# Optimization experiments

Measured on AMD Instinct MI355X. Metric: run time of the kernel, lower is better.

The kernel has to match this reference:

```python
import jax, jax.numpy as jnp
import numpy as np
from jax import lax

KH = 5
KW = 5


def dwconv3x3(x, w, b):
    # depthwise 3x3, padding 1; w: (C,1,3,3), b: (C,)
    C = x.shape[1]
    y = lax.conv_general_dilated(x, w, (1, 1), ((1, 1), (1, 1)),
                                 feature_group_count=C,
                                 dimension_numbers=('NCHW', 'OIHW', 'NCHW'))
    return y + b[None, :, None, None]


def conv3x3(x, w, b):
    y = lax.conv_general_dilated(x, w, (1, 1), ((1, 1), (1, 1)),
                                 dimension_numbers=('NCHW', 'OIHW', 'NCHW'))
    return y + b[None, :, None, None]


def resize_bilinear_ac(x, H, W):
    # bilinear, align_corners=True (matches F.interpolate(..., align_corners=True))
    N, C, h, w = x.shape
    ys = jnp.linspace(0.0, h - 1.0, H)
    xs = jnp.linspace(0.0, w - 1.0, W)
    y0 = jnp.floor(ys).astype(jnp.int32)
    x0 = jnp.floor(xs).astype(jnp.int32)
    y1 = jnp.clip(y0 + 1, 0, h - 1)
    x1 = jnp.clip(x0 + 1, 0, w - 1)
    wy = (ys - y0)[None, None, :, None]
    wx = (xs - x0)[None, None, None, :]
    rows = x[:, :, y0, :] * (1.0 - wy) + x[:, :, y1, :] * wy  # (N,C,H,w)
    out = rows[:, :, :, x0] * (1.0 - wx) + rows[:, :, :, x1] * wx  # (N,C,H,W)
    return out


def unfold_kxk(x, kH, kW):
    # torch.nn.Unfold(kernel=(kH,kW), padding=(kH//2,kW//2)) reshaped to (N,C,kH*kW,H,W)
    N, C, H, W = x.shape
    ph, pw = kH // 2, kW // 2
    xp = jnp.pad(x, ((0, 0), (0, 0), (ph, ph), (pw, pw)))
    patches = [xp[:, :, i:i + H, j:j + W] for i in range(kH) for j in range(kW)]
    return jnp.stack(patches, axis=2)  # (N,C,kH*kW,H,W), row-major window order


def setup_inputs() -> dict:
    key = jax.random.key(0)
    ks = jax.random.split(key, 11)
    N, C, H, W = 2, 128, 128, 128
    s = 1.0 / np.sqrt(9.0)
    return {
        'hr_feat': jax.random.normal(ks[0], (N, C, H, W), jnp.float32),
        'lr_feat': jax.random.normal(ks[1], (N, C, H // 2, W // 2), jnp.float32),
        'wq': jax.random.normal(ks[2], (C, 1, 3, 3), jnp.float32) * s,
        'bq': jax.random.normal(ks[3], (C,), jnp.float32) * 0.02,
        'wk': jax.random.normal(ks[4], (C, 1, 3, 3), jnp.float32) * s,
        'bk': jax.random.normal(ks[5], (C,), jnp.float32) * 0.02,
        'wv': jax.random.normal(ks[6], (C, 1, 3, 3), jnp.float32) * s,
        'bv': jax.random.normal(ks[7], (C,), jnp.float32) * 0.02,
        'wa': jax.random.normal(ks[8], (2, 2 * C, 3, 3), jnp.float32) * (1.0 / np.sqrt(9.0 * 2 * C)),
        'ba': jax.random.normal(ks[9], (2,), jnp.float32) * 0.02,
    }


def reference(hr_feat, lr_feat, wq, bq, wk, bk, wv, bv, wa, ba):
    N, C, H, W = hr_feat.shape
    lr_up = resize_bilinear_ac(lr_feat, H, W)
    hr_value = dwconv3x3(hr_feat, wv, bv)
    hr_key = dwconv3x3(hr_feat, wk, bk)
    lr_query = dwconv3x3(lr_up, wq, bq)
    fused = jnp.concatenate([lr_query, hr_key], axis=1)
    dyn = jax.nn.sigmoid(conv3x3(fused, wa, ba))  # (N,2,H,W)
    k_unf = unfold_kxk(hr_key, KH, KW)            # (N,C,K,H,W)
    sim = jnp.einsum('nchw,nckhw->nkhw', lr_query, k_unf)
    weight = jax.nn.softmax(sim, axis=1)          # softmax over window K
    v_unf = unfold_kxk(hr_value, KH, KW)
    attn = dyn[:, 0:1] * jnp.einsum('nckhw,nkhw->nchw', v_unf, weight)
    attn = attn + dyn[:, 1:2] * hr_value
    return lr_up + attn
```

## Files before the change

### kernel.cpp

```cpp
#include <hip/hip_runtime.h>
#include <hip/hip_fp16.h>
#include <math.h>

constexpr int C  = 128;
constexpr int H  = 128;
constexpr int Wd = 128;
constexpr int HW = H * Wd;
constexpr int LH = 64, LW = 64;
constexpr int CP = 64;

constexpr int KRW = 136;
constexpr int KPLANE = 132 * KRW;
constexpr int QRW = 136;
constexpr int QPLANE = 130 * QRW;
constexpr int KSZ = 2 * CP * KPLANE;
constexpr int QSZ = 2 * CP * QPLANE;
constexpr int LSZ = 2 * CP * HW;
constexpr int WAHSZ = 2304;

typedef _Float16 __attribute__((ext_vector_type(2))) v2h;

#if __has_builtin(__builtin_amdgcn_fdot2)
#define DOT2(a, b, c) __builtin_amdgcn_fdot2((a), (b), (c), false)
#else
#define DOT2(a, b, c) ((c) + (float)(a).x * (float)(b).x + (float)(a).y * (float)(b).y)
#endif

struct __attribute__((packed, aligned(4)))  f4u { float x, y, z, w; };
struct __attribute__((packed, aligned(4)))  f4p { v2h a, b, c, d; };
struct __attribute__((packed, aligned(8)))  h2x2 { v2h a, b; };
struct __attribute__((packed, aligned(16))) h4 { v2h a, b, c, d; };

__device__ __forceinline__ v2h pack2(float a, float b) {
  v2h r; r.x = (_Float16)a; r.y = (_Float16)b; return r;
}

__global__ __launch_bounds__(256) void k_pre(
    const float* __restrict__ hr, const float* __restrict__ lr,
    const float* __restrict__ wq, const float* __restrict__ bq,
    const float* __restrict__ wk, const float* __restrict__ bk,
    const float* __restrict__ wv, const float* __restrict__ bv,
    const float* __restrict__ wa,
    v2h* __restrict__ qpad, v2h* __restrict__ kpad, v2h* __restrict__ vpad,
    v2h* __restrict__ lrup, v2h* __restrict__ zgapA, v2h* __restrict__ zgapB,
    v2h* __restrict__ wah)
{
  const int B   = blockIdx.x;
  const int tid = threadIdx.x;
  const int t   = B * 256 + tid;
  const int q   = B & 7;
  const int m   = B >> 3;
  const int j   = (q << 1) | (m & 1);
  const int ncp = m >> 1;
  const int x4  = tid & 31;
  const int y   = (j << 3) | ((tid >> 5) & 7);
  const int x   = x4 * 4;
  const int cp  = ncp & (CP - 1);
  const int n   = ncp >> 6;
  const int c0  = cp * 2;
  const v2h hz  = pack2(0.f, 0.f);
  h4 Z; Z.a = hz; Z.b = hz; Z.c = hz; Z.d = hz;

  if (t < WAHSZ) {
    const int cpw = t / 36, r = t - cpw * 36;
    const int o = r / 18, s2 = (r - o * 18) / 9, tap = r - o * 18 - s2 * 9;
    const int c = s2 * 128 + 2 * cpw;
    wah[t] = pack2(wa[(o * 256 + c) * 9 + tap], wa[(o * 256 + c + 1) * 9 + tap]);
  }

  float ko[2][4], vo[2][4];
#pragma unroll
  for (int cc = 0; cc < 2; cc++) {
    const int c = c0 + cc;
    const float* hp = hr + (n * C + c) * HW;
    const float* wkc = wk + c * 9;
    const float* wvc = wv + c * 9;
    const float bkc = bk[c], bvc = bv[c];
#pragma unroll
    for (int jj = 0; jj < 4; jj++) { ko[cc][jj] = bkc; vo[cc][jj] = bvc; }
#pragma unroll
    for (int r = 0; r < 3; r++) {
      const int gy = y + r - 1;
      const bool okr = (gy >= 0) && (gy < H);
      const int gyc = min(max(gy, 0), H - 1);
      const float* rp = hp + gyc * Wd;
      const f4u mm = *(const f4u*)(rp + x);
      const float lft = rp[max(x - 1, 0)];
      const float rgt = rp[min(x + 4, Wd - 1)];
      float h[6];
      h[0] = (okr && x > 0) ? lft : 0.f;
      h[1] = okr ? mm.x : 0.f;  h[2] = okr ? mm.y : 0.f;
      h[3] = okr ? mm.z : 0.f;  h[4] = okr ? mm.w : 0.f;
      h[5] = (okr && x + 4 < Wd) ? rgt : 0.f;
#pragma unroll
      for (int dj = 0; dj < 3; dj++) {
        const float a = wkc[r * 3 + dj], b = wvc[r * 3 + dj];
#pragma unroll
        for (int jj = 0; jj < 4; jj++) {
          ko[cc][jj] += a * h[jj + dj];
          vo[cc][jj] += b * h[jj + dj];
        }
      }
    }
  }

  v2h* kr = kpad + ncp * KPLANE + (y + 2) * KRW + 4 + x;
  v2h* vr = vpad + ncp * KPLANE + (y + 2) * KRW + 4 + x;
  {
    h4 K4; K4.a = pack2(ko[0][0], ko[1][0]); K4.b = pack2(ko[0][1], ko[1][1]);
           K4.c = pack2(ko[0][2], ko[1][2]); K4.d = pack2(ko[0][3], ko[1][3]);
    h4 V4; V4.a = pack2(vo[0][0], vo[1][0]); V4.b = pack2(vo[0][1], vo[1][1]);
           V4.c = pack2(vo[0][2], vo[1][2]); V4.d = pack2(vo[0][3], vo[1][3]);
    *(h4*)(kr) = K4;
    *(h4*)(vr) = V4;
  }

  const float s = 63.0f / 127.0f;

  float rwm[3][3]; int rA[3];
  {
    int ry0[3]; float wyv[3]; bool okr[3];
#pragma unroll
    for (int r = 0; r < 3; r++) {
      const int gy = y + r - 1;
      okr[r] = (gy >= 0) && (gy < H);
      const int gyc = min(max(gy, 0), H - 1);
      const float fy = gyc * s;
      const int y0 = (int)fy;
      ry0[r] = y0;
      wyv[r] = fy - y0;
    }
    const int Y = ry0[0];
#pragma unroll
    for (int tt = 0; tt < 3; tt++) rA[tt] = min(Y + tt, LH - 1) * LW;
#pragma unroll
    for (int r = 0; r < 3; r++) {
      const int i0 = ry0[r] - Y;
      const int i1 = min(ry0[r] + 1, LH - 1) - Y;
#pragma unroll
      for (int tt = 0; tt < 3; tt++) {
        const float w = ((tt == i0) ? (1.f - wyv[r]) : 0.f)
                      + ((tt == i1) ? wyv[r] : 0.f);
        rwm[r][tt] = okr[r] ? w : 0.f;
      }
    }
  }

  float cwm[6][5]; int XB;
  {
    int cx0[6]; float wxv[6]; bool okc[6];
#pragma unroll
    for (int jj = 0; jj < 6; jj++) {
      const int gx = x + jj - 1;
      okc[jj] = (gx >= 0) && (gx < Wd);
      const int gxc = min(max(gx, 0), Wd - 1);
      const float fx = gxc * s;
      const int x0 = (int)fx;
      cx0[jj] = x0;
      wxv[jj] = fx - x0;
    }
    XB = min(cx0[0], LW - 5);
#pragma unroll
    for (int jj = 0; jj < 6; jj++) {
      const int i0 = cx0[jj] - XB;
      const int i1 = min(cx0[jj] + 1, LW - 1) - XB;
#pragma unroll
      for (int u = 0; u < 5; u++) {
        const float w = ((u == i0) ? (1.f - wxv[jj]) : 0.f)
                      + ((u == i1) ? wxv[jj] : 0.f);
        cwm[jj][u] = okc[jj] ? w : 0.f;
      }
    }
  }

  float qo[2][4], up[2][4];
#pragma unroll
  for (int cc = 0; cc < 2; cc++) {
    const int c = c0 + cc;
    const float* lp = lr + (n * C + c) * (LH * LW);
    const float* wqc = wq + c * 9;
    const float bqc = bq[c];
#pragma unroll
    for (int jj = 0; jj < 4; jj++) qo[cc][jj] = bqc;

    float R[3][5];
#pragma unroll
    for (int tt = 0; tt < 3; tt++) {
      const f4u mm = *(const f4u*)(lp + rA[tt] + XB);
      R[tt][0] = mm.x; R[tt][1] = mm.y; R[tt][2] = mm.z; R[tt][3] = mm.w;
      R[tt][4] = lp[rA[tt] + XB + 4];
    }

    float yi[3][5];
#pragma unroll
    for (int r = 0; r < 3; r++)
#pragma unroll
      for (int u = 0; u < 5; u++)
        yi[r][u] = rwm[r][0] * R[0][u] + rwm[r][1] * R[1][u]
                 + rwm[r][2] * R[2][u];

#pragma unroll
    for (int r = 0; r < 3; r++) {
      float row[6];
#pragma unroll
      for (int jj = 0; jj < 6; jj++)
        row[jj] = cwm[jj][0] * yi[r][0] + cwm[jj][1] * yi[r][1]
               + cwm[jj][2] * yi[r][2] + cwm[jj][3] * yi[r][3]
               + cwm[jj][4] * yi[r][4];
#pragma unroll
      for (int dj = 0; dj < 3; dj++) {
        const float a = wqc[r * 3 + dj];
#pragma unroll
        for (int jj = 0; jj < 4; jj++) qo[cc][jj] += a * row[jj + dj];
      }
      if (r == 1) {
        up[cc][0] = row[1]; up[cc][1] = row[2];
        up[cc][2] = row[3]; up[cc][3] = row[4];
      }
    }
  }

  {
    h4 U;
    U.a = pack2(up[0][0], up[1][0]); U.b = pack2(up[0][1], up[1][1]);
    U.c = pack2(up[0][2], up[1][2]); U.d = pack2(up[0][3], up[1][3]);
    *(h4*)(lrup + ncp * HW + y * Wd + x) = U;
  }
  v2h* qr = qpad + ncp * QPLANE + (y + 1) * QRW + 4 + x;
  {
    h4 Q4; Q4.a = pack2(qo[0][0], qo[1][0]); Q4.b = pack2(qo[0][1], qo[1][1]);
           Q4.c = pack2(qo[0][2], qo[1][2]); Q4.d = pack2(qo[0][3], qo[1][3]);
    *(h4*)(qr) = Q4;
  }

  if (x4 == 0) {
    *(h4*)(kr - 4) = Z; *(h4*)(vr - 4) = Z; *(h4*)(qr - 4) = Z;
  }
  if (x4 == 31) {
    *(h4*)(kr + 4) = Z; *(h4*)(vr + 4) = Z; *(h4*)(qr + 4) = Z;
  }
  if (y == 0) {
    v2h* kz = kpad + ncp * KPLANE;
    v2h* vz = vpad + ncp * KPLANE;
    v2h* qz = qpad + ncp * QPLANE;
    *(h4*)(kz + 4 + x) = Z; *(h4*)(kz + KRW + 4 + x) = Z;
    *(h4*)(vz + 4 + x) = Z; *(h4*)(vz + KRW + 4 + x) = Z;
    *(h4*)(qz + 4 + x) = Z;
    if (x4 == 0) {
      *(h4*)(kz) = Z; *(h4*)(kz + KRW) = Z;
      *(h4*)(vz) = Z; *(h4*)(vz + KRW) = Z;
      *(h4*)(qz) = Z;
    }
    if (x4 == 31) {
      *(h4*)(kz + 132) = Z; *(h4*)(kz + KRW + 132) = Z;
      *(h4*)(vz + 132) = Z; *(h4*)(vz + KRW + 132) = Z;
      *(h4*)(qz + 132) = Z;
    }
  }
  if (y == 127) {
    v2h* kz = kpad + ncp * KPLANE + 130 * KRW;
    v2h* vz = vpad + ncp * KPLANE + 130 * KRW;
    v2h* qz = qpad + ncp * QPLANE + 129 * QRW;
    *(h4*)(kz + 4 + x) = Z; *(h4*)(kz + KRW + 4 + x) = Z;
    *(h4*)(vz + 4 + x) = Z; *(h4*)(vz + KRW + 4 + x) = Z;
    *(h4*)(qz + 4 + x) = Z;
    if (x4 == 0) {
      *(h4*)(kz) = Z; *(h4*)(kz + KRW) = Z;
      *(h4*)(vz) = Z; *(h4*)(vz + KRW) = Z;
      *(h4*)(qz) = Z;
    }
    if (x4 == 31) {
      *(h4*)(kz + 132) = Z; *(h4*)(kz + KRW + 132) = Z;
      *(h4*)(vz + 132) = Z; *(h4*)(vz + KRW + 132) = Z;
      *(h4*)(qz + 132) = Z;
    }
  }
  if (t < 256) zgapA[t] = hz;
  if (t < 4)   zgapB[t] = hz;
}

#define DECLK(P, kp) \
  const f4p P##A0 = *(const f4p*)(kp); \
  const f4p P##A1 = *(const f4p*)((kp) + KRW); \
  const f4p P##A2 = *(const f4p*)((kp) + 2 * KRW); \
  const f4p P##A3 = *(const f4p*)((kp) + 3 * KRW); \
  const f4p P##A4 = *(const f4p*)((kp) + 4 * KRW); \
  const v2h P##b0 = (kp)[4]; \
  const v2h P##b1 = (kp)[KRW + 4]; \
  const v2h P##b2 = (kp)[2 * KRW + 4]; \
  const v2h P##b3 = (kp)[3 * KRW + 4]; \
  const v2h P##b4 = (kp)[4 * KRW + 4];

#define DECLQ(P, qp) \
  const f4p P##Q0 = *(const f4p*)(qp); \
  const f4p P##Q1 = *(const f4p*)((qp) + QRW); \
  const f4p P##Q2 = *(const f4p*)((qp) + 2 * QRW);

#define SIM25(P, qc) \
  sim[0]  = DOT2(qc, P##A0.a, sim[0]);  sim[1]  = DOT2(qc, P##A0.b, sim[1]); \
  sim[2]  = DOT2(qc, P##A0.c, sim[2]);  sim[3]  = DOT2(qc, P##A0.d, sim[3]); \
  sim[4]  = DOT2(qc, P##b0,   sim[4]); \
  sim[5]  = DOT2(qc, P##A1.a, sim[5]);  sim[6]  = DOT2(qc, P##A1.b, sim[6]); \
  sim[7]  = DOT2(qc, P##A1.c, sim[7]);  sim[8]  = DOT2(qc, P##A1.d, sim[8]); \
  sim[9]  = DOT2(qc, P##b1,   sim[9]); \
  sim[10] = DOT2(qc, P##A2.a, sim[10]); sim[11] = DOT2(qc, P##A2.b, sim[11]); \
  sim[12] = DOT2(qc, P##A2.c, sim[12]); sim[13] = DOT2(qc, P##A2.d, sim[13]); \
  sim[14] = DOT2(qc, P##b2,   sim[14]); \
  sim[15] = DOT2(qc, P##A3.a, sim[15]); sim[16] = DOT2(qc, P##A3.b, sim[16]); \
  sim[17] = DOT2(qc, P##A3.c, sim[17]); sim[18] = DOT2(qc, P##A3.d, sim[18]); \
  sim[19] = DOT2(qc, P##b3,   sim[19]); \
  sim[20] = DOT2(qc, P##A4.a, sim[20]); sim[21] = DOT2(qc, P##A4.b, sim[21]); \
  sim[22] = DOT2(qc, P##A4.c, sim[22]); sim[23] = DOT2(qc, P##A4.d, sim[23]); \
  sim[24] = DOT2(qc, P##b4,   sim[24]);

#define GATE(P, wp) { \
  const v2h q3_[9] = {P##Q0.a, P##Q0.b, P##Q0.c, P##Q1.a, P##Q1.b, P##Q1.c, \
                      P##Q2.a, P##Q2.b, P##Q2.c}; \
  const v2h k3_[9] = {P##A1.b, P##A1.c, P##A1.d, P##A2.b, P##A2.c, P##A2.d, \
                      P##A3.b, P##A3.c, P##A3.d}; \
  _Pragma("unroll") \
  for (int tp = 0; tp < 9; tp++) { \
    d0a = DOT2((wp)[tp],      q3_[tp], d0a); \
    d0a = DOT2((wp)[9 + tp],  k3_[tp], d0a); \
    d1a = DOT2((wp)[18 + tp], q3_[tp], d1a); \
    d1a = DOT2((wp)[27 + tp], k3_[tp], d1a); \
  } }

#define EPI(P, ci) { \
  v2h accA = wpk[0] * P##A0.a; \
  accA += wpk[1]  * P##A0.b;  accA += wpk[2]  * P##A0.c; \
  accA += wpk[3]  * P##A0.d;  accA += wpk[4]  * P##b0; \
  v2h accB = wpk[5] * P##A1.a; \
  accB += wpk[6]  * P##A1.b;  accB += wpk[7]  * P##A1.c; \
  accB += wpk[8]  * P##A1.d;  accB += wpk[9]  * P##b1; \
  accA += wpk[10] * P##A2.a;  accA += wpk[11] * P##A2.b; \
  accA += wpk[12] * P##A2.c;  accA += wpk[13] * P##A2.d; \
  accA += wpk[14] * P##b2; \
  accB += wpk[15] * P##A3.a;  accB += wpk[16] * P##A3.b; \
  accB += wpk[17] * P##A3.c;  accB += wpk[18] * P##A3.d; \
  accB += wpk[19] * P##b3; \
  accA += wpk[20] * P##A4.a;  accA += wpk[21] * P##A4.b; \
  accA += wpk[22] * P##A4.c;  accA += wpk[23] * P##A4.d; \
  accA += wpk[24] * P##b4; \
  const float acc0 = (float)accA.x + (float)accB.x; \
  const float acc1 = (float)accA.y + (float)accB.y; \
  const v2h vc = P##A2.c; \
  const v2h lu = lub[(ci) * HW]; \
  float* op = opb + (ci) * 2 * HW; \
  op[0]  = (float)lu.x + g0 * acc0 + g1 * (float)vc.x; \
  op[HW] = (float)lu.y + g0 * acc1 + g1 * (float)vc.y; }

__global__ __launch_bounds__(1024, 4) void k_attn(
    const v2h* __restrict__ qpad, const v2h* __restrict__ kpad,
    const v2h* __restrict__ vpad, const v2h* __restrict__ lrup,
    const v2h* __restrict__ wah, const float* __restrict__ ba,
    float* __restrict__ outb)
{
  __shared__ float red[25 * 1024];
  __shared__ float dsh[2 * 1024];

  const int tid = threadIdx.x;
  const int px  = tid & 63;
  const int cgu = __builtin_amdgcn_readfirstlane((tid >> 6) & 7);
  const int row = __builtin_amdgcn_readfirstlane(tid >> 9);
  const int slot = blockIdx.x;
  const int xcd = slot & 7;
  const int m   = slot >> 3;
  const int y   = (xcd << 4) + ((m & 7) << 1) + row;
  const int x   = ((m >> 3) & 1) * 64 + px;
  const int n   = m >> 4;
  const int cp0 = cgu * 8;

  const float ba0 = ba[0], ba1 = ba[1];

  const v2h* kb = kpad + (n * CP + cp0) * KPLANE + y * KRW + 2 + x;
  const v2h* qb = qpad + (n * CP + cp0) * QPLANE + y * QRW + 3 + x;

  float sim[25];
#pragma unroll
  for (int k = 0; k < 25; k++) sim[k] = 0.f;
  float d0a = 0.f, d1a = 0.f;

#pragma unroll
  for (int cib = 0; cib < 8; cib += 2) {
    const v2h* kp0 = kb + cib * KPLANE;
    const v2h* kp1 = kp0 + KPLANE;
    const v2h* qp0 = qb + cib * QPLANE;
    const v2h* qp1 = qp0 + QPLANE;

    DECLK(S, kp0)
    DECLK(T, kp1)
    DECLQ(S, qp0)

    const v2h qc0 = SQ1.b;
    SIM25(S, qc0)
    GATE(S, wah + (cp0 + cib) * 36)

    DECLQ(T, qp1)
    const v2h qc1 = TQ1.b;
    SIM25(T, qc1)
    GATE(T, wah + (cp0 + cib + 1) * 36)
  }

#pragma unroll
  for (int k = 0; k < 25; k++) red[k * 1024 + tid] = sim[k];
  dsh[tid] = d0a;
  dsh[1024 + tid] = d1a;
  __syncthreads();

  {
    const int w = tid >> 6;
    for (int s = w; s < 54; s += 16) {
      if (s < 50) {
        const int k = s >> 1, r = s & 1;
        float acc = 0.f;
#pragma unroll
        for (int g = 0; g < 8; g++) acc += red[k * 1024 + r * 512 + g * 64 + px];
        red[k * 1024 + r * 512 + px] = acc;
      } else {
        const int jj = s - 50;
        const int r = jj & 1, which = jj >> 1;
        float acc = 0.f;
#pragma unroll
        for (int g = 0; g < 8; g++) acc += dsh[which * 1024 + r * 512 + g * 64 + px];
        dsh[which * 1024 + r * 512 + px] = acc;
      }
    }
  }
  __syncthreads();

  const v2h* vb = vpad + (n * CP + cp0) * KPLANE + y * KRW + 2 + x;
  const v2h* lub = lrup + (n * CP + cp0) * HW + y * Wd + x;
  float* opb = outb + (n * C + 2 * cp0) * HW + y * Wd + x;

  DECLK(VA, vb)
  DECLK(VB, vb + KPLANE)

  const int rbase = row * 512 + px;
  float w[25];
  float mx = -1e30f;
#pragma unroll
  for (int k = 0; k < 25; k++) { w[k] = red[k * 1024 + rbase]; mx = fmaxf(mx, w[k]); }
  float tot = 0.f;
#pragma unroll
  for (int k = 0; k < 25; k++) { const float e = __expf(w[k] - mx); w[k] = e; tot += e; }
  const float inv = __builtin_amdgcn_rcpf(tot);
  v2h wpk[25];
#pragma unroll
  for (int k = 0; k < 25; k++) {
    const float wf = w[k] * inv;
    wpk[k] = pack2(wf, wf);
  }
  const float g0 = __builtin_amdgcn_rcpf(1.f + __expf(-(dsh[rbase] + ba0)));
  const float g1 = __builtin_amdgcn_rcpf(1.f + __expf(-(dsh[1024 + rbase] + ba1)));

  EPI(VA, 0)
  EPI(VB, 1)

#pragma unroll
  for (int cib = 2; cib < 8; cib += 2) {
    DECLK(VC, vb + cib * KPLANE)
    DECLK(VD, vb + (cib + 1) * KPLANE)
    EPI(VC, cib)
    EPI(VD, cib + 1)
  }
}

extern "C" void kernel_launch(void* const* d_in, const int* in_sizes, int n_in,
                              void* d_out, int out_size, void* d_ws,
                              size_t ws_size, hipStream_t stream)
{
  const float* hr = (const float*)d_in[0];
  const float* lr = (const float*)d_in[1];
  const float* wq = (const float*)d_in[2];
  const float* bq = (const float*)d_in[3];
  const float* wk = (const float*)d_in[4];
  const float* bk = (const float*)d_in[5];
  const float* wv = (const float*)d_in[6];
  const float* bv = (const float*)d_in[7];
  const float* wa = (const float*)d_in[8];
  const float* ba = (const float*)d_in[9];

  float* out = (float*)d_out;
  v2h* ws2 = (v2h*)d_ws;

  v2h* kpad  = ws2;
  v2h* vpad  = kpad + KSZ;
  v2h* qpad  = vpad + KSZ;
  v2h* zgapA = qpad + QSZ;
  v2h* lrupb = zgapA + 256;
  v2h* zgapB = lrupb + LSZ;
  v2h* wahb  = zgapB + 4;

  k_pre<<<dim3(2048), dim3(256), 0, stream>>>(
      hr, lr, wq, bq, wk, bk, wv, bv, wa,
      qpad, kpad, vpad, lrupb, zgapA, zgapB, wahb);
  k_attn<<<dim3(256), dim3(1024), 0, stream>>>(
      qpad, kpad, vpad, lrupb, wahb, ba, out);
}
```

Before: 118.1 us.

## Fuse key/value depthwise convs into attention kernel via shared-memory staging

Removes the key and value depthwise 3x3 convolutions from the pre-pass and their padded fp16 global buffers. The attention kernel now computes them directly from hr into an LDS tile with halo, first for keys and then for values, reusing the same buffer. The cross-channel-group reduction of sim and gate partials now uses LDS atomicAdd into a small buffer instead of a large staging array and a tree pass. This cuts global writes and reads of the K/V intermediates. In exchange, each block recomputes halo rows and columns, and the conv work plus atomic contention now sit inside the attention kernel's critical path.

```diff
diff --git a/kernel.cpp b/kernel.cpp
--- a/kernel.cpp
+++ b/kernel.cpp
@@ -9,14 +9,13 @@
 constexpr int LH = 64, LW = 64;
 constexpr int CP = 64;
 
-constexpr int KRW = 136;
-constexpr int KPLANE = 132 * KRW;
 constexpr int QRW = 136;
 constexpr int QPLANE = 130 * QRW;
-constexpr int KSZ = 2 * CP * KPLANE;
 constexpr int QSZ = 2 * CP * QPLANE;
 constexpr int LSZ = 2 * CP * HW;
 constexpr int WAHSZ = 2304;
+
+constexpr int KVSTR = 433;
 
 typedef _Float16 __attribute__((ext_vector_type(2))) v2h;
 
@@ -28,7 +27,6 @@
 
 struct __attribute__((packed, aligned(4)))  f4u { float x, y, z, w; };
 struct __attribute__((packed, aligned(4)))  f4p { v2h a, b, c, d; };
-struct __attribute__((packed, aligned(8)))  h2x2 { v2h a, b; };
 struct __attribute__((packed, aligned(16))) h4 { v2h a, b, c, d; };
 
 __device__ __forceinline__ v2h pack2(float a, float b) {
@@ -36,13 +34,11 @@
 }
 
 __global__ __launch_bounds__(256) void k_pre(
-    const float* __restrict__ hr, const float* __restrict__ lr,
+    const float* __restrict__ lr,
     const float* __restrict__ wq, const float* __restrict__ bq,
-    const float* __restrict__ wk, const float* __restrict__ bk,
-    const float* __restrict__ wv, const float* __restrict__ bv,
     const float* __restrict__ wa,
-    v2h* __restrict__ qpad, v2h* __restrict__ kpad, v2h* __restrict__ vpad,
-    v2h* __restrict__ lrup, v2h* __restrict__ zgapA, v2h* __restrict__ zgapB,
+    v2h* __restrict__ qpad, v2h* __restrict__ lrup,
+    v2h* __restrict__ zgapA, v2h* __restrict__ zgapB,
     v2h* __restrict__ wah)
 {
   const int B   = blockIdx.x;
@@ -68,53 +64,6 @@
     wah[t] = pack2(wa[(o * 256 + c) * 9 + tap], wa[(o * 256 + c + 1) * 9 + tap]);
   }
 
-  float ko[2][4], vo[2][4];
-#pragma unroll
-  for (int cc = 0; cc < 2; cc++) {
-    const int c = c0 + cc;
-    const float* hp = hr + (n * C + c) * HW;
-    const float* wkc = wk + c * 9;
-    const float* wvc = wv + c * 9;
-    const float bkc = bk[c], bvc = bv[c];
-#pragma unroll
-    for (int jj = 0; jj < 4; jj++) { ko[cc][jj] = bkc; vo[cc][jj] = bvc; }
-#pragma unroll
-    for (int r = 0; r < 3; r++) {
-      const int gy = y + r - 1;
-      const bool okr = (gy >= 0) && (gy < H);
-      const int gyc = min(max(gy, 0), H - 1);
-      const float* rp = hp + gyc * Wd;
-      const f4u mm = *(const f4u*)(rp + x);
-      const float lft = rp[max(x - 1, 0)];
-      const float rgt = rp[min(x + 4, Wd - 1)];
-      float h[6];
-      h[0] = (okr && x > 0) ? lft : 0.f;
-      h[1] = okr ? mm.x : 0.f;  h[2] = okr ? mm.y : 0.f;
-      h[3] = okr ? mm.z : 0.f;  h[4] = okr ? mm.w : 0.f;
-      h[5] = (okr && x + 4 < Wd) ? rgt : 0.f;
-#pragma unroll
-      for (int dj = 0; dj < 3; dj++) {
-        const float a = wkc[r * 3 + dj], b = wvc[r * 3 + dj];
-#pragma unroll
-        for (int jj = 0; jj < 4; jj++) {
-          ko[cc][jj] += a * h[jj + dj];
-          vo[cc][jj] += b * h[jj + dj];
-        }
-      }
-    }
-  }
-
-  v2h* kr = kpad + ncp * KPLANE + (y + 2) * KRW + 4 + x;
-  v2h* vr = vpad + ncp * KPLANE + (y + 2) * KRW + 4 + x;
-  {
-    h4 K4; K4.a = pack2(ko[0][0], ko[1][0]); K4.b = pack2(ko[0][1], ko[1][1]);
-           K4.c = pack2(ko[0][2], ko[1][2]); K4.d = pack2(ko[0][3], ko[1][3]);
-    h4 V4; V4.a = pack2(vo[0][0], vo[1][0]); V4.b = pack2(vo[0][1], vo[1][1]);
-           V4.c = pack2(vo[0][2], vo[1][2]); V4.d = pack2(vo[0][3], vo[1][3]);
-    *(h4*)(kr) = K4;
-    *(h4*)(vr) = V4;
-  }
-
   const float s = 63.0f / 127.0f;
 
   float rwm[3][3]; int rA[3];
@@ -233,63 +182,33 @@
     *(h4*)(qr) = Q4;
   }
 
-  if (x4 == 0) {
-    *(h4*)(kr - 4) = Z; *(h4*)(vr - 4) = Z; *(h4*)(qr - 4) = Z;
-  }
-  if (x4 == 31) {
-    *(h4*)(kr + 4) = Z; *(h4*)(vr + 4) = Z; *(h4*)(qr + 4) = Z;
-  }
+  if (x4 == 0)  { *(h4*)(qr - 4) = Z; }
+  if (x4 == 31) { *(h4*)(qr + 4) = Z; }
   if (y == 0) {
-    v2h* kz = kpad + ncp * KPLANE;
-    v2h* vz = vpad + ncp * KPLANE;
     v2h* qz = qpad + ncp * QPLANE;
-    *(h4*)(kz + 4 + x) = Z; *(h4*)(kz + KRW + 4 + x) = Z;
-    *(h4*)(vz + 4 + x) = Z; *(h4*)(vz + KRW + 4 + x) = Z;
     *(h4*)(qz + 4 + x) = Z;
-    if (x4 == 0) {
-      *(h4*)(kz) = Z; *(h4*)(kz + KRW) = Z;
-      *(h4*)(vz) = Z; *(h4*)(vz + KRW) = Z;
-      *(h4*)(qz) = Z;
-    }
-    if (x4 == 31) {
-      *(h4*)(kz + 132) = Z; *(h4*)(kz + KRW + 132) = Z;
-      *(h4*)(vz + 132) = Z; *(h4*)(vz + KRW + 132) = Z;
-      *(h4*)(qz + 132) = Z;
-    }
+    if (x4 == 0)  { *(h4*)(qz) = Z; }
+    if (x4 == 31) { *(h4*)(qz + 132) = Z; }
   }
   if (y == 127) {
-    v2h* kz = kpad + ncp * KPLANE + 130 * KRW;
-    v2h* vz = vpad + ncp * KPLANE + 130 * KRW;
     v2h* qz = qpad + ncp * QPLANE + 129 * QRW;
-    *(h4*)(kz + 4 + x) = Z; *(h4*)(kz + KRW + 4 + x) = Z;
-    *(h4*)(vz + 4 + x) = Z; *(h4*)(vz + KRW + 4 + x) = Z;
     *(h4*)(qz + 4 + x) = Z;
-    if (x4 == 0) {
-      *(h4*)(kz) = Z; *(h4*)(kz + KRW) = Z;
-      *(h4*)(vz) = Z; *(h4*)(vz + KRW) = Z;
-      *(h4*)(qz) = Z;
-    }
-    if (x4 == 31) {
-      *(h4*)(kz + 132) = Z; *(h4*)(kz + KRW + 132) = Z;
-      *(h4*)(vz + 132) = Z; *(h4*)(vz + KRW + 132) = Z;
-      *(h4*)(qz + 132) = Z;
-    }
+    if (x4 == 0)  { *(h4*)(qz) = Z; }
+    if (x4 == 31) { *(h4*)(qz + 132) = Z; }
   }
   if (t < 256) zgapA[t] = hz;
   if (t < 4)   zgapB[t] = hz;
 }
 
-#define DECLK(P, kp) \
-  const f4p P##A0 = *(const f4p*)(kp); \
-  const f4p P##A1 = *(const f4p*)((kp) + KRW); \
-  const f4p P##A2 = *(const f4p*)((kp) + 2 * KRW); \
-  const f4p P##A3 = *(const f4p*)((kp) + 3 * KRW); \
-  const f4p P##A4 = *(const f4p*)((kp) + 4 * KRW); \
-  const v2h P##b0 = (kp)[4]; \
-  const v2h P##b1 = (kp)[KRW + 4]; \
-  const v2h P##b2 = (kp)[2 * KRW + 4]; \
-  const v2h P##b3 = (kp)[3 * KRW + 4]; \
-  const v2h P##b4 = (kp)[4 * KRW + 4];
+#define DECLK_L(P, kb_) \
+  f4p P##A0, P##A1, P##A2, P##A3, P##A4; \
+  v2h P##b0, P##b1, P##b2, P##b3, P##b4; \
+  { const v2h* kp_ = (kb_); \
+    P##A0.a = kp_[0];   P##A0.b = kp_[1];   P##A0.c = kp_[2];   P##A0.d = kp_[3];   P##b0 = kp_[4]; \
+    P##A1.a = kp_[72];  P##A1.b = kp_[73];  P##A1.c = kp_[74];  P##A1.d = kp_[75];  P##b1 = kp_[76]; \
+    P##A2.a = kp_[144]; P##A2.b = kp_[145]; P##A2.c = kp_[146]; P##A2.d = kp_[147]; P##b2 = kp_[148]; \
+    P##A3.a = kp_[216]; P##A3.b = kp_[217]; P##A3.c = kp_[218]; P##A3.d = kp_[219]; P##b3 = kp_[220]; \
+    P##A4.a = kp_[288]; P##A4.b = kp_[289]; P##A4.c = kp_[290]; P##A4.d = kp_[291]; P##b4 = kp_[292]; }
 
 #define DECLQ(P, qp) \
   const f4p P##Q0 = *(const f4p*)(qp); \
@@ -350,119 +269,163 @@
   op[0]  = (float)lu.x + g0 * acc0 + g1 * (float)vc.x; \
   op[HW] = (float)lu.y + g0 * acc1 + g1 * (float)vc.y; }
 
+__device__ __forceinline__ void stage_conv(
+    v2h* kvt, const float* __restrict__ hr,
+    const float* __restrict__ wc, const float* __restrict__ bc,
+    int n, int y0, int x0, int tid)
+{
+  const v2h hz = pack2(0.f, 0.f);
+  for (int jb = tid; jb < 1536; jb += 1024) {
+    const int cp = jb & 63;
+    const int rest = jb >> 6;
+    const int r = rest >> 2;
+    const int chunk = rest & 3;
+    const int gy = y0 - 2 + r;
+    v2h* dst = kvt + cp * KVSTR + r * 72 + chunk * 17;
+    if (gy < 0 || gy >= H) {
+#pragma unroll
+      for (int t = 0; t < 17; t++) dst[t] = hz;
+      continue;
+    }
+    const int gc = x0 - 2 + chunk * 17;
+    const bool fast = (gc >= 1) && (gc <= 110);
+    float o[2][17];
+#pragma unroll
+    for (int cc = 0; cc < 2; cc++) {
+      const int c = 2 * cp + cc;
+      const float* hp = hr + (n * C + c) * HW;
+      const float* wcc = wc + c * 9;
+      float w9[9];
+#pragma unroll
+      for (int i = 0; i < 9; i++) w9[i] = wcc[i];
+      const float bcc = bc[c];
+#pragma unroll
+      for (int t = 0; t < 17; t++) o[cc][t] = bcc;
+#pragma unroll
+      for (int rr = 0; rr < 3; rr++) {
+        const int gyr = gy - 1 + rr;
+        if (gyr >= 0 && gyr < H) {
+          const float* rp = hp + gyr * Wd;
+          float rv[19];
+          if (fast) {
+            const f4u m0 = *(const f4u*)(rp + gc - 1);
+            const f4u m1 = *(const f4u*)(rp + gc + 3);
+            const f4u m2 = *(const f4u*)(rp + gc + 7);
+            const f4u m3 = *(const f4u*)(rp + gc + 11);
+            const f4u m4 = *(const f4u*)(rp + gc + 14);
+            rv[0]=m0.x;  rv[1]=m0.y;  rv[2]=m0.z;  rv[3]=m0.w;
+            rv[4]=m1.x;  rv[5]=m1.y;  rv[6]=m1.z;  rv[7]=m1.w;
+            rv[8]=m2.x;  rv[9]=m2.y;  rv[10]=m2.z; rv[11]=m2.w;
+            rv[12]=m3.x; rv[13]=m3.y; rv[14]=m3.z; rv[15]=m3.w;
+            rv[16]=m4.y; rv[17]=m4.z; rv[18]=m4.w;
+          } else {
+#pragma unroll
+            for (int k2 = 0; k2 < 19; k2++) {
+              const int col = gc - 1 + k2;
+              rv[k2] = (col >= 0 && col < Wd) ? rp[col] : 0.f;
+            }
+          }
+#pragma unroll
+          for (int jt = 0; jt < 3; jt++) {
+            const float wj = w9[rr * 3 + jt];
+#pragma unroll
+            for (int t = 0; t < 17; t++) o[cc][t] += wj * rv[t + jt];
+          }
+        }
+      }
+    }
+#pragma unroll
+    for (int t = 0; t < 17; t++) {
+      const int oc = gc + t;
+      dst[t] = (oc >= 0 && oc < Wd) ? pack2(o[0][t], o[1][t]) : hz;
+    }
+  }
+}
+
 __global__ __launch_bounds__(1024, 4) void k_attn(
-    const v2h* __restrict__ qpad, const v2h* __restrict__ kpad,
-    const v2h* __restrict__ vpad, const v2h* __restrict__ lrup,
+    const float* __restrict__ hr,
+    const v2h* __restrict__ qpad, const v2h* __restrict__ lrup,
     const v2h* __restrict__ wah, const float* __restrict__ ba,
+    const float* __restrict__ wk, const float* __restrict__ bk,
+    const float* __restrict__ wv, const float* __restrict__ bv,
     float* __restrict__ outb)
 {
-  __shared__ float red[25 * 1024];
-  __shared__ float dsh[2 * 1024];
+  __shared__ v2h kvt[64 * KVSTR];
+  __shared__ float accd[27 * 128];
 
   const int tid = threadIdx.x;
   const int px  = tid & 63;
-  const int cgu = __builtin_amdgcn_readfirstlane((tid >> 6) & 7);
-  const int row = __builtin_amdgcn_readfirstlane(tid >> 9);
+  const int w   = tid >> 6;
+  const int cgu = __builtin_amdgcn_readfirstlane(w & 7);
+  const int row = __builtin_amdgcn_readfirstlane(w >> 3);
   const int slot = blockIdx.x;
   const int xcd = slot & 7;
   const int m   = slot >> 3;
-  const int y   = (xcd << 4) + ((m & 7) << 1) + row;
-  const int x   = ((m >> 3) & 1) * 64 + px;
+  const int y0  = (xcd << 4) + ((m & 7) << 1);
+  const int y   = y0 + row;
+  const int x0  = ((m >> 3) & 1) * 64;
+  const int x   = x0 + px;
   const int n   = m >> 4;
   const int cp0 = cgu * 8;
 
   const float ba0 = ba[0], ba1 = ba[1];
 
-  const v2h* kb = kpad + (n * CP + cp0) * KPLANE + y * KRW + 2 + x;
+  for (int i = tid; i < 27 * 128; i += 1024) accd[i] = 0.f;
+  stage_conv(kvt, hr, wk, bk, n, y0, x0, tid);
+  __syncthreads();
+
   const v2h* qb = qpad + (n * CP + cp0) * QPLANE + y * QRW + 3 + x;
-
   float sim[25];
 #pragma unroll
   for (int k = 0; k < 25; k++) sim[k] = 0.f;
   float d0a = 0.f, d1a = 0.f;
 
 #pragma unroll
-  for (int cib = 0; cib < 8; cib += 2) {
-    const v2h* kp0 = kb + cib * KPLANE;
-    const v2h* kp1 = kp0 + KPLANE;
-    const v2h* qp0 = qb + cib * QPLANE;
-    const v2h* qp1 = qp0 + QPLANE;
-
-    DECLK(S, kp0)
-    DECLK(T, kp1)
-    DECLQ(S, qp0)
-
-    const v2h qc0 = SQ1.b;
-    SIM25(S, qc0)
+  for (int cib = 0; cib < 8; cib++) {
+    const v2h* kb_ = kvt + (cp0 + cib) * KVSTR + row * 72 + px;
+    DECLK_L(S, kb_)
+    const v2h* qp_ = qb + cib * QPLANE;
+    DECLQ(S, qp_)
+    const v2h qc = SQ1.b;
+    SIM25(S, qc)
     GATE(S, wah + (cp0 + cib) * 36)
-
-    DECLQ(T, qp1)
-    const v2h qc1 = TQ1.b;
-    SIM25(T, qc1)
-    GATE(T, wah + (cp0 + cib + 1) * 36)
-  }
-
-#pragma unroll
-  for (int k = 0; k < 25; k++) red[k * 1024 + tid] = sim[k];
-  dsh[tid] = d0a;
-  dsh[1024 + tid] = d1a;
+  }
+
+  const int rb = (row << 6) + px;
+#pragma unroll
+  for (int k = 0; k < 25; k++) atomicAdd(&accd[k * 128 + rb], sim[k]);
+  atomicAdd(&accd[25 * 128 + rb], d0a);
+  atomicAdd(&accd[26 * 128 + rb], d1a);
   __syncthreads();
 
-  {
-    const int w = tid >> 6;
-    for (int s = w; s < 54; s += 16) {
-      if (s < 50) {
-        const int k = s >> 1, r = s & 1;
-        float acc = 0.f;
-#pragma unroll
-        for (int g = 0; g < 8; g++) acc += red[k * 1024 + r * 512 + g * 64 + px];
-        red[k * 1024 + r * 512 + px] = acc;
-      } else {
-        const int jj = s - 50;
-        const int r = jj & 1, which = jj >> 1;
-        float acc = 0.f;
-#pragma unroll
-        for (int g = 0; g < 8; g++) acc += dsh[which * 1024 + r * 512 + g * 64 + px];
-        dsh[which * 1024 + r * 512 + px] = acc;
-      }
-    }
-  }
+  stage_conv(kvt, hr, wv, bv, n, y0, x0, tid);
+
+  float wf[25];
+  float mx = -1e30f;
+#pragma unroll
+  for (int k = 0; k < 25; k++) { wf[k] = accd[k * 128 + rb]; mx = fmaxf(mx, wf[k]); }
+  float tot = 0.f;
+#pragma unroll
+  for (int k = 0; k < 25; k++) { const float e = __expf(wf[k] - mx); wf[k] = e; tot += e; }
+  const float inv = __builtin_amdgcn_rcpf(tot);
+  v2h wpk[25];
+#pragma unroll
+  for (int k = 0; k < 25; k++) {
+    const float ww = wf[k] * inv;
+    wpk[k] = pack2(ww, ww);
+  }
+  const float g0 = __builtin_amdgcn_rcpf(1.f + __expf(-(accd[25 * 128 + rb] + ba0)));
+  const float g1 = __builtin_amdgcn_rcpf(1.f + __expf(-(accd[26 * 128 + rb] + ba1)));
   __syncthreads();
 
-  const v2h* vb = vpad + (n * CP + cp0) * KPLANE + y * KRW + 2 + x;
   const v2h* lub = lrup + (n * CP + cp0) * HW + y * Wd + x;
   float* opb = outb + (n * C + 2 * cp0) * HW + y * Wd + x;
 
-  DECLK(VA, vb)
-  DECLK(VB, vb + KPLANE)
-
-  const int rbase = row * 512 + px;
-  float w[25];
-  float mx = -1e30f;
-#pragma unroll
-  for (int k = 0; k < 25; k++) { w[k] = red[k * 1024 + rbase]; mx = fmaxf(mx, w[k]); }
-  float tot = 0.f;
-#pragma unroll
-  for (int k = 0; k < 25; k++) { const float e = __expf(w[k] - mx); w[k] = e; tot += e; }
-  const float inv = __builtin_amdgcn_rcpf(tot);
-  v2h wpk[25];
-#pragma unroll
-  for (int k = 0; k < 25; k++) {
-    const float wf = w[k] * inv;
-    wpk[k] = pack2(wf, wf);
-  }
-  const float g0 = __builtin_amdgcn_rcpf(1.f + __expf(-(dsh[rbase] + ba0)));
-  const float g1 = __builtin_amdgcn_rcpf(1.f + __expf(-(dsh[1024 + rbase] + ba1)));
-
-  EPI(VA, 0)
-  EPI(VB, 1)
-
-#pragma unroll
-  for (int cib = 2; cib < 8; cib += 2) {
-    DECLK(VC, vb + cib * KPLANE)
-    DECLK(VD, vb + (cib + 1) * KPLANE)
-    EPI(VC, cib)
-    EPI(VD, cib + 1)
+#pragma unroll
+  for (int cib = 0; cib < 8; cib++) {
+    const v2h* kb_ = kvt + (cp0 + cib) * KVSTR + row * 72 + px;
+    DECLK_L(E, kb_)
+    EPI(E, cib)
   }
 }
 
@@ -484,17 +447,14 @@
   float* out = (float*)d_out;
   v2h* ws2 = (v2h*)d_ws;
 
-  v2h* kpad  = ws2;
-  v2h* vpad  = kpad + KSZ;
-  v2h* qpad  = vpad + KSZ;
+  v2h* qpad  = ws2;
   v2h* zgapA = qpad + QSZ;
   v2h* lrupb = zgapA + 256;
   v2h* zgapB = lrupb + LSZ;
   v2h* wahb  = zgapB + 4;
 
   k_pre<<<dim3(2048), dim3(256), 0, stream>>>(
-      hr, lr, wq, bq, wk, bk, wv, bv, wa,
-      qpad, kpad, vpad, lrupb, zgapA, zgapB, wahb);
+      lr, wq, bq, wa, qpad, lrupb, zgapA, zgapB, wahb);
   k_attn<<<dim3(256), dim3(1024), 0, stream>>>(
-      qpad, kpad, vpad, lrupb, wahb, ba, out);
+      hr, qpad, lrupb, wahb, ba, wk, bk, wv, bv, out);
 }
```

New measurement: 198.8 us. +68.3%, slower.
